# Performance work log

Measured on AMD Instinct MI355X. Metric: run time of the kernel, lower is better.

The kernel has to match this reference:

```python
import jax, jax.numpy as jnp
import numpy as np

N_NODES = 100000
N_EDGES = 1600000
D = 128

def setup_inputs() -> dict:
    key = jax.random.key(0)
    k1, k2, k3, k4 = jax.random.split(key, 4)
    x = jax.random.normal(k1, (N_NODES, D), dtype=jnp.float32)
    edge_index = jax.random.randint(k2, (2, N_EDGES), 0, N_NODES, dtype=jnp.int64)
    eps = jnp.zeros((1,), dtype=jnp.float32)
    W1 = jax.random.normal(k3, (D, D), dtype=jnp.float32) * (1.0 / np.sqrt(D))
    b1 = jnp.zeros((D,), dtype=jnp.float32)
    W2 = jax.random.normal(k4, (D, D), dtype=jnp.float32) * (1.0 / np.sqrt(D))
    b2 = jnp.zeros((D,), dtype=jnp.float32)
    return {"x": x, "edge_index": edge_index, "eps": eps,
            "W1": W1, "b1": b1, "W2": W2, "b2": b2}

def reference(x, edge_index, eps, W1, b1, W2, b2):
    src, dst = edge_index[0], edge_index[1]
    # spmm: sum of neighbor features h_j for each destination node i
    agg = jax.ops.segment_sum(x[src], dst, num_segments=N_NODES)  # [N, D]
    out = (1.0 + eps[0]) * x + agg
    # apply_func: 2-layer MLP (GIN paper)
    h = jax.nn.relu(out @ W1 + b1)
    return h @ W2 + b2
```

## Files before the change

### kernel.cpp

```cpp
#include <hip/hip_runtime.h>

#define D 128
#define BSHIFT 7
#define NSUB 8
#define SUBCAP 384
#define CAP 2560
#define LDSPITCH 136

#define NBMAX 784
#define LCAP 16
#define FCH 8
#define NBIN 256

typedef __attribute__((ext_vector_type(8))) short bf16x8;
typedef __attribute__((ext_vector_type(4))) float f32x4;
typedef __attribute__((ext_vector_type(2))) float f32x2;
typedef __attribute__((ext_vector_type(4))) unsigned int u32x4;

__device__ __forceinline__ unsigned short f2bf(float f) {
    union { float f; unsigned int u; } c; c.f = f;
    return (unsigned short)((c.u + 0x7FFFu + ((c.u >> 16) & 1u)) >> 16);
}

__global__ __launch_bounds__(512) void zerocur(int* __restrict__ cur, int ncur)
{
    int gid = blockIdx.x * 512 + threadIdx.x;
    if (gid < ncur) cur[gid] = 0;
}

__global__ __launch_bounds__(512) void conv_bin(
    const float* __restrict__ x, unsigned short* __restrict__ xb,
    const float* __restrict__ W1, unsigned short* __restrict__ W1t,
    const float* __restrict__ W2, unsigned short* __restrict__ W2t,
    const int* __restrict__ ei, int* __restrict__ cur,
    int* __restrict__ pairs, int E, int nbuck, int total4)
{
    __shared__ int lbuf[NBMAX * LCAP];
    __shared__ int lcnt[NBMAX];

    int tid = threadIdx.x;

    if (blockIdx.x >= NBIN) {
        int base = (blockIdx.x - NBIN) * 1024 + tid;
        #pragma unroll
        for (int t = 0; t < 2; ++t) {
            int gid = base + t * 512;
            if (gid < total4) {
                float4 v = ((const float4*)x)[gid];
                ushort4 o;
                o.x = f2bf(v.x); o.y = f2bf(v.y);
                o.z = f2bf(v.z); o.w = f2bf(v.w);
                ((ushort4*)xb)[gid] = o;
            } else {
                int r = gid - total4;
                if (r < 16384) {
                    int n = r >> 7, k = r & 127;
                    W1t[n * 128 + k] = f2bf(W1[k * 128 + n]);
                } else {
                    r -= 16384;
                    if (r < 16384) {
                        int n = r >> 7, k = r & 127;
                        W2t[n * 128 + k] = f2bf(W2[k * 128 + n]);
                    }
                }
            }
        }
        return;
    }

    int slice = blockIdx.x & (NSUB - 1);
    int epb = (E + NBIN - 1) / NBIN;
    int start = blockIdx.x * epb;
    int end = min(start + epb, E);

    for (int b = tid; b < nbuck; b += 512) lcnt[b] = 0;
    __syncthreads();

    for (int base = start; base < end; base += 512) {
        int gid = base + tid;
        if (gid < end) {
            int d = __builtin_nontemporal_load(&ei[E + gid]);
            int s = __builtin_nontemporal_load(&ei[gid]);
            int b = d >> BSHIFT;
            int val = ((d & 127) << 17) | s;
            int pos = atomicAdd(&lcnt[b], 1);
            if (pos < LCAP) {
                lbuf[b * LCAP + pos] = val;
            } else {
                int sb = b * NSUB + slice;
                int gp = atomicAdd(&cur[sb], 1);
                if (gp < SUBCAP) pairs[(size_t)sb * SUBCAP + gp] = val;
            }
        }
        __syncthreads();
        for (int b = tid; b < nbuck; b += 512) {
            int c = min(lcnt[b], LCAP);
            int nf = (c / FCH) * FCH;
            if (nf > 0) {
                int sb = b * NSUB + slice;
                int gbase = atomicAdd(&cur[sb], nf);
                int* dst = pairs + (size_t)sb * SUBCAP + gbase;
                if ((gbase & 3) == 0 && gbase + nf <= SUBCAP) {
                    #pragma unroll
                    for (int i = 0; i < LCAP; i += 4) {
                        if (i >= nf) break;
                        *(int4*)(dst + i) = *(int4*)(lbuf + b * LCAP + i);
                    }
                } else {
                    for (int i = 0; i < nf; ++i)
                        if (gbase + i < SUBCAP) dst[i] = lbuf[b * LCAP + i];
                }
                int rem = c - nf;
                for (int i = 0; i < rem; ++i)
                    lbuf[b * LCAP + i] = lbuf[b * LCAP + nf + i];
                lcnt[b] = rem;
            } else {
                lcnt[b] = c;
            }
        }
        __syncthreads();
    }

    for (int b = tid; b < nbuck; b += 512) {
        int c = min(lcnt[b], LCAP);
        if (c > 0) {
            int sb = b * NSUB + slice;
            int gbase = atomicAdd(&cur[sb], c);
            for (int i = 0; i < c; ++i)
                if (gbase + i < SUBCAP)
                    pairs[(size_t)sb * SUBCAP + gbase + i] = lbuf[b * LCAP + i];
        }
    }
}

__global__ __launch_bounds__(256) void local_fill(
    const int* __restrict__ cur, const int* __restrict__ pairs,
    int* __restrict__ csr, int* __restrict__ rs, int N)
{
    __shared__ int ldata[CAP];
    __shared__ int outsrc[CAP];
    __shared__ int lcnt[128], lofs[128], lincl[128];
    __shared__ int red[256];

    int b = blockIdx.x;
    int tid = threadIdx.x;
    int node0 = b << BSHIFT;

    int pacc = 0;
    for (int i = tid; i < b * NSUB; i += 256) pacc += min(cur[i], SUBCAP);
    red[tid] = pacc;
    __syncthreads();
    for (int s = 128; s > 0; s >>= 1) {
        if (tid < s) red[tid] += red[tid + s];
        __syncthreads();
    }
    int base = red[0];

    int off = 0;
    #pragma unroll
    for (int s = 0; s < NSUB; ++s) {
        int c = min(cur[b * NSUB + s], SUBCAP);
        const int* pp = pairs + (size_t)(b * NSUB + s) * SUBCAP;
        for (int i = tid; i < c && off + i < CAP; i += 256)
            ldata[off + i] = pp[i];
        off += c;
    }
    int cnt = min(off, CAP);
    __syncthreads();

    if (tid < 128) lcnt[tid] = 0;
    __syncthreads();
    for (int i = tid; i < cnt; i += 256)
        atomicAdd(&lcnt[ldata[i] >> 17], 1);
    __syncthreads();

    if (tid < 128) lincl[tid] = lcnt[tid];
    __syncthreads();
    for (int off2 = 1; off2 < 128; off2 <<= 1) {
        int t = 0;
        if (tid < 128 && tid >= off2) t = lincl[tid - off2];
        __syncthreads();
        if (tid < 128) lincl[tid] += t;
        __syncthreads();
    }
    if (tid < 128) lofs[tid] = lincl[tid] - lcnt[tid];
    __syncthreads();

    for (int i = tid; i < cnt; i += 256) {
        int v = ldata[i];
        int p = atomicAdd(&lofs[v >> 17], 1);
        outsrc[p] = v & 0x1FFFF;
    }
    __syncthreads();

    for (int i = tid; i < cnt; i += 256)
        csr[base + i] = outsrc[i];
    int nn = N - node0; if (nn > 128) nn = 128;
    if (tid < nn) rs[node0 + tid] = base + lincl[tid];
}

__global__ __launch_bounds__(256, 3) void mlp_gather(
    const unsigned short* __restrict__ xb, const float* __restrict__ epsp,
    const int* __restrict__ rs, const int* __restrict__ csr,
    const unsigned short* __restrict__ W1t, const float* __restrict__ b1,
    const unsigned short* __restrict__ W2t, const float* __restrict__ b2,
    float* __restrict__ out, int N)
{
    __shared__ unsigned short Wl[128 * LDSPITCH];
    __shared__ unsigned short Al[64 * LDSPITCH];

    int tid = threadIdx.x;
    int row0 = blockIdx.x * 64;

    for (int i = tid; i < 128 * 16; i += 256) {
        int r = i >> 4, cc = i & 15;
        ((int4*)(Wl + r * LDSPITCH))[cc] = ((const int4*)(W1t + r * 128))[cc];
    }

    {
        int sub  = tid >> 5;
        int lane = threadIdx.x & 31;
        int hi   = lane >> 4;
        int c16  = lane & 15;
        int boff = c16 * 8;
        float ep1 = 1.0f + epsp[0];

        for (int nn = 0; nn < 8; ++nn) {
            int r = nn * 8 + sub;
            int node = row0 + r;
            if (node >= N) {
                if (hi == 0) {
                    u32x4 z = {0u, 0u, 0u, 0u};
                    *(u32x4*)(Al + r * LDSPITCH + boff) = z;
                }
                continue;
            }
            int start = (node == 0) ? 0 : rs[node - 1];
            int end   = rs[node];

            f32x2 acc[4];
            {
                u32x4 xr = *(const u32x4*)(xb + (size_t)node * D + boff);
                f32x2 z2 = {0.f, 0.f};
                #pragma unroll
                for (int e = 0; e < 4; ++e) {
                    unsigned int w = xr[e];
                    f32x2 t;
                    t.x = __uint_as_float(w << 16);
                    t.y = __uint_as_float(w & 0xFFFF0000u);
                    acc[e] = hi ? z2 : (ep1 * t);
                }
            }

            #define ACC8(v)                                                 \
                {                                                           \
                    _Pragma("unroll")                                       \
                    for (int e = 0; e < 4; ++e) {                           \
                        unsigned int w = (v)[e];                            \
                        f32x2 t;                                            \
                        t.x = __uint_as_float(w << 16);                     \
                        t.y = __uint_as_float(w & 0xFFFF0000u);             \
                        acc[e] += t;                                        \
                    }                                                       \
                }

            int j = start;
            for (; j + 8 <= end; j += 8) {
                int i0 = csr[j + hi],     i1 = csr[j + 2 + hi];
                int i2 = csr[j + 4 + hi], i3 = csr[j + 6 + hi];
                u32x4 v0 = *(const u32x4*)(xb + (size_t)i0 * D + boff);
                u32x4 v1 = *(const u32x4*)(xb + (size_t)i1 * D + boff);
                u32x4 v2 = *(const u32x4*)(xb + (size_t)i2 * D + boff);
                u32x4 v3 = *(const u32x4*)(xb + (size_t)i3 * D + boff);
                ACC8(v0); ACC8(v1); ACC8(v2); ACC8(v3);
            }
            if (j < end) {
                int lim = end - 1;
                int e0 = j + hi, e1 = j + 2 + hi;
                int e2 = j + 4 + hi, e3 = j + 6 + hi;
                int s0 = csr[min(e0, lim)], s1 = csr[min(e1, lim)];
                int s2 = csr[min(e2, lim)], s3 = csr[min(e3, lim)];
                u32x4 v0 = *(const u32x4*)(xb + (size_t)s0 * D + boff);
                u32x4 v1 = *(const u32x4*)(xb + (size_t)s1 * D + boff);
                u32x4 v2 = *(const u32x4*)(xb + (size_t)s2 * D + boff);
                u32x4 v3 = *(const u32x4*)(xb + (size_t)s3 * D + boff);
                unsigned int m0 = (e0 < end) ? 0xFFFFFFFFu : 0u;
                unsigned int m1 = (e1 < end) ? 0xFFFFFFFFu : 0u;
                unsigned int m2 = (e2 < end) ? 0xFFFFFFFFu : 0u;
                unsigned int m3 = (e3 < end) ? 0xFFFFFFFFu : 0u;
                #pragma unroll
                for (int e = 0; e < 4; ++e) {
                    v0[e] &= m0; v1[e] &= m1; v2[e] &= m2; v3[e] &= m3;
                }
                ACC8(v0); ACC8(v1); ACC8(v2); ACC8(v3);
            }
            #undef ACC8

            #pragma unroll
            for (int e = 0; e < 4; ++e) {
                acc[e].x += __shfl_xor(acc[e].x, 16);
                acc[e].y += __shfl_xor(acc[e].y, 16);
            }

            if (hi == 0) {
                u32x4 o;
                #pragma unroll
                for (int e = 0; e < 4; ++e) {
                    unsigned int lo = f2bf(acc[e].x);
                    unsigned int hf = f2bf(acc[e].y);
                    o[e] = lo | (hf << 16);
                }
                *(u32x4*)(Al + r * LDSPITCH + boff) = o;
            }
        }
    }
    __syncthreads();

    int wave = tid >> 6, lane = tid & 63;
    int l16 = lane & 15, lq = lane >> 4;

    f32x4 acc[8];
    #pragma unroll
    for (int t = 0; t < 8; ++t) acc[t] = (f32x4){0.f, 0.f, 0.f, 0.f};

    int arow = wave * 16 + l16;
    #pragma unroll
    for (int kk = 0; kk < 4; ++kk) {
        int k0 = kk * 32 + lq * 8;
        bf16x8 a = *(const bf16x8*)(Al + arow * LDSPITCH + k0);
        #pragma unroll
        for (int t = 0; t < 8; ++t) {
            bf16x8 b = *(const bf16x8*)(Wl + (t * 16 + l16) * LDSPITCH + k0);
            acc[t] = __builtin_amdgcn_mfma_f32_16x16x32_bf16(a, b, acc[t], 0, 0, 0);
        }
    }
    __syncthreads();

    for (int i = tid; i < 128 * 16; i += 256) {
        int r = i >> 4, cc = i & 15;
        ((int4*)(Wl + r * LDSPITCH))[cc] = ((const int4*)(W2t + r * 128))[cc];
    }
    #pragma unroll
    for (int t = 0; t < 8; ++t) {
        int col = t * 16 + l16;
        float bv = b1[col];
        #pragma unroll
        for (int r = 0; r < 4; ++r) {
            int row = wave * 16 + lq * 4 + r;
            float v = fmaxf(acc[t][r] + bv, 0.0f);
            Al[row * LDSPITCH + col] = f2bf(v);
        }
    }
    __syncthreads();

    #pragma unroll
    for (int t = 0; t < 8; ++t) acc[t] = (f32x4){0.f, 0.f, 0.f, 0.f};
    #pragma unroll
    for (int kk = 0; kk < 4; ++kk) {
        int k0 = kk * 32 + lq * 8;
        bf16x8 a = *(const bf16x8*)(Al + arow * LDSPITCH + k0);
        #pragma unroll
        for (int t = 0; t < 8; ++t) {
            bf16x8 b = *(const bf16x8*)(Wl + (t * 16 + l16) * LDSPITCH + k0);
            acc[t] = __builtin_amdgcn_mfma_f32_16x16x32_bf16(a, b, acc[t], 0, 0, 0);
        }
    }

    #pragma unroll
    for (int t = 0; t < 8; ++t) {
        int col = t * 16 + l16;
        float bv = b2[col];
        #pragma unroll
        for (int r = 0; r < 4; ++r) {
            int row = row0 + wave * 16 + lq * 4 + r;
            if (row >= N) continue;
            out[(size_t)row * 128 + col] = acc[t][r] + bv;
        }
    }
}

extern "C" void kernel_launch(void* const* d_in, const int* in_sizes, int n_in,
                              void* d_out, int out_size, void* d_ws, size_t ws_size,
                              hipStream_t stream) {
    const float* x   = (const float*)d_in[0];
    const int*   ei  = (const int*)d_in[1];
    const float* eps = (const float*)d_in[2];
    const float* W1  = (const float*)d_in[3];
    const float* b1  = (const float*)d_in[4];
    const float* W2  = (const float*)d_in[5];
    const float* b2  = (const float*)d_in[6];
    float* out = (float*)d_out;

    int E = in_sizes[1] / 2;
    int N = in_sizes[0] / D;
    int nbuck = (N + 127) >> BSHIFT;
    int ncur = nbuck * NSUB;

    char* ws = (char*)d_ws;
    int* cur   = (int*)(ws);
    int* rs    = (int*)(ws + 32768);
    int* pairs = (int*)(ws + 434176);
    int* csr   = (int*)(ws + 10044416);
    unsigned short* xb  = (unsigned short*)(ws + 16445440);
    unsigned short* W1t = (unsigned short*)(ws + 67647488);
    unsigned short* W2t = (unsigned short*)(ws + 67680256);

    int total4 = N * D / 4;
    int convitems = total4 + 32768;
    int nconv = (convitems + 1023) / 1024;

    zerocur<<<(ncur + 511) / 512, 512, 0, stream>>>(cur, ncur);
    conv_bin<<<NBIN + nconv, 512, 0, stream>>>(
        x, xb, W1, W1t, W2, W2t, ei, cur, pairs, E, nbuck, total4);
    local_fill<<<nbuck, 256, 0, stream>>>(cur, pairs, csr, rs, N);

    int gemm_blocks = (N + 63) / 64;
    mlp_gather<<<gemm_blocks, 256, 0, stream>>>(
        xb, eps, rs, csr, W1t, b1, W2t, b2, out, N);
}
```

Before: 256.5 us.

## Double threads per gather-MLP block and unroll neighbor gather to sixteen edges

The fused gather+MLP kernel now runs 512 threads per 64-row block instead of 256. Each 32-lane group handles 4 nodes instead of 8, and the two MFMA passes are split so each wave computes half the output columns. The neighbor gather loop is unrolled to 16 edges per iteration to keep more loads in flight. This aims to raise memory-level parallelism in the latency-bound gather, at the cost of more register pressure under launch_bounds(512,4) and fewer MFMAs per wave.

```diff
diff --git a/kernel.cpp b/kernel.cpp
--- a/kernel.cpp
+++ b/kernel.cpp
@@ -199,7 +199,7 @@
     if (tid < nn) rs[node0 + tid] = base + lincl[tid];
 }
 
-__global__ __launch_bounds__(256, 3) void mlp_gather(
+__global__ __launch_bounds__(512, 4) void mlp_gather512(
     const unsigned short* __restrict__ xb, const float* __restrict__ epsp,
     const int* __restrict__ rs, const int* __restrict__ csr,
     const unsigned short* __restrict__ W1t, const float* __restrict__ b1,
@@ -212,21 +212,21 @@
     int tid = threadIdx.x;
     int row0 = blockIdx.x * 64;
 
-    for (int i = tid; i < 128 * 16; i += 256) {
+    for (int i = tid; i < 128 * 16; i += 512) {
         int r = i >> 4, cc = i & 15;
         ((int4*)(Wl + r * LDSPITCH))[cc] = ((const int4*)(W1t + r * 128))[cc];
     }
 
     {
         int sub  = tid >> 5;
-        int lane = threadIdx.x & 31;
+        int lane = tid & 31;
         int hi   = lane >> 4;
         int c16  = lane & 15;
         int boff = c16 * 8;
         float ep1 = 1.0f + epsp[0];
 
-        for (int nn = 0; nn < 8; ++nn) {
-            int r = nn * 8 + sub;
+        for (int nn = 0; nn < 4; ++nn) {
+            int r = nn * 16 + sub;
             int node = row0 + r;
             if (node >= N) {
                 if (hi == 0) {
@@ -265,7 +265,23 @@
                 }
 
             int j = start;
-            for (; j + 8 <= end; j += 8) {
+            for (; j + 16 <= end; j += 16) {
+                int i0 = csr[j      + hi], i1 = csr[j +  2 + hi];
+                int i2 = csr[j +  4 + hi], i3 = csr[j +  6 + hi];
+                int i4 = csr[j +  8 + hi], i5 = csr[j + 10 + hi];
+                int i6 = csr[j + 12 + hi], i7 = csr[j + 14 + hi];
+                u32x4 v0 = *(const u32x4*)(xb + (size_t)i0 * D + boff);
+                u32x4 v1 = *(const u32x4*)(xb + (size_t)i1 * D + boff);
+                u32x4 v2 = *(const u32x4*)(xb + (size_t)i2 * D + boff);
+                u32x4 v3 = *(const u32x4*)(xb + (size_t)i3 * D + boff);
+                u32x4 v4 = *(const u32x4*)(xb + (size_t)i4 * D + boff);
+                u32x4 v5 = *(const u32x4*)(xb + (size_t)i5 * D + boff);
+                u32x4 v6 = *(const u32x4*)(xb + (size_t)i6 * D + boff);
+                u32x4 v7 = *(const u32x4*)(xb + (size_t)i7 * D + boff);
+                ACC8(v0); ACC8(v1); ACC8(v2); ACC8(v3);
+                ACC8(v4); ACC8(v5); ACC8(v6); ACC8(v7);
+            }
+            if (j + 8 <= end) {
                 int i0 = csr[j + hi],     i1 = csr[j + 2 + hi];
                 int i2 = csr[j + 4 + hi], i3 = csr[j + 6 + hi];
                 u32x4 v0 = *(const u32x4*)(xb + (size_t)i0 * D + boff);
@@ -273,6 +289,7 @@
                 u32x4 v2 = *(const u32x4*)(xb + (size_t)i2 * D + boff);
                 u32x4 v3 = *(const u32x4*)(xb + (size_t)i3 * D + boff);
                 ACC8(v0); ACC8(v1); ACC8(v2); ACC8(v3);
+                j += 8;
             }
             if (j < end) {
                 int lim = end - 1;
@@ -318,63 +335,67 @@
 
     int wave = tid >> 6, lane = tid & 63;
     int l16 = lane & 15, lq = lane >> 4;
-
-    f32x4 acc[8];
-    #pragma unroll
-    for (int t = 0; t < 8; ++t) acc[t] = (f32x4){0.f, 0.f, 0.f, 0.f};
-
-    int arow = wave * 16 + l16;
+    int g = wave >> 1;
+    int h = wave & 1;
+    int arow = g * 16 + l16;
+
+    f32x4 acc[4];
+    #pragma unroll
+    for (int t = 0; t < 4; ++t) acc[t] = (f32x4){0.f, 0.f, 0.f, 0.f};
+
     #pragma unroll
     for (int kk = 0; kk < 4; ++kk) {
         int k0 = kk * 32 + lq * 8;
         bf16x8 a = *(const bf16x8*)(Al + arow * LDSPITCH + k0);
         #pragma unroll
-        for (int t = 0; t < 8; ++t) {
+        for (int tt = 0; tt < 4; ++tt) {
+            int t = h * 4 + tt;
             bf16x8 b = *(const bf16x8*)(Wl + (t * 16 + l16) * LDSPITCH + k0);
-            acc[t] = __builtin_amdgcn_mfma_f32_16x16x32_bf16(a, b, acc[t], 0, 0, 0);
-        }
-    }
-    __syncthreads();
-
-    for (int i = tid; i < 128 * 16; i += 256) {
+            acc[tt] = __builtin_amdgcn_mfma_f32_16x16x32_bf16(a, b, acc[tt], 0, 0, 0);
+        }
+    }
+    __syncthreads();
+
+    for (int i = tid; i < 128 * 16; i += 512) {
         int r = i >> 4, cc = i & 15;
         ((int4*)(Wl + r * LDSPITCH))[cc] = ((const int4*)(W2t + r * 128))[cc];
     }
     #pragma unroll
-    for (int t = 0; t < 8; ++t) {
-        int col = t * 16 + l16;
+    for (int tt = 0; tt < 4; ++tt) {
+        int col = (h * 4 + tt) * 16 + l16;
         float bv = b1[col];
         #pragma unroll
         for (int r = 0; r < 4; ++r) {
-            int row = wave * 16 + lq * 4 + r;
-            float v = fmaxf(acc[t][r] + bv, 0.0f);
+            int row = g * 16 + lq * 4 + r;
+            float v = fmaxf(acc[tt][r] + bv, 0.0f);
             Al[row * LDSPITCH + col] = f2bf(v);
         }
     }
     __syncthreads();
 
     #pragma unroll
-    for (int t = 0; t < 8; ++t) acc[t] = (f32x4){0.f, 0.f, 0.f, 0.f};
+    for (int t = 0; t < 4; ++t) acc[t] = (f32x4){0.f, 0.f, 0.f, 0.f};
     #pragma unroll
     for (int kk = 0; kk < 4; ++kk) {
         int k0 = kk * 32 + lq * 8;
         bf16x8 a = *(const bf16x8*)(Al + arow * LDSPITCH + k0);
         #pragma unroll
-        for (int t = 0; t < 8; ++t) {
+        for (int tt = 0; tt < 4; ++tt) {
+            int t = h * 4 + tt;
             bf16x8 b = *(const bf16x8*)(Wl + (t * 16 + l16) * LDSPITCH + k0);
-            acc[t] = __builtin_amdgcn_mfma_f32_16x16x32_bf16(a, b, acc[t], 0, 0, 0);
-        }
-    }
-
-    #pragma unroll
-    for (int t = 0; t < 8; ++t) {
-        int col = t * 16 + l16;
+            acc[tt] = __builtin_amdgcn_mfma_f32_16x16x32_bf16(a, b, acc[tt], 0, 0, 0);
+        }
+    }
+
+    #pragma unroll
+    for (int tt = 0; tt < 4; ++tt) {
+        int col = (h * 4 + tt) * 16 + l16;
         float bv = b2[col];
         #pragma unroll
         for (int r = 0; r < 4; ++r) {
-            int row = row0 + wave * 16 + lq * 4 + r;
+            int row = row0 + g * 16 + lq * 4 + r;
             if (row >= N) continue;
-            out[(size_t)row * 128 + col] = acc[t][r] + bv;
+            out[(size_t)row * 128 + col] = acc[tt][r] + bv;
         }
     }
 }
@@ -415,6 +436,6 @@
     local_fill<<<nbuck, 256, 0, stream>>>(cur, pairs, csr, rs, N);
 
     int gemm_blocks = (N + 63) / 64;
-    mlp_gather<<<gemm_blocks, 256, 0, stream>>>(
+    mlp_gather512<<<gemm_blocks, 512, 0, stream>>>(
         xb, eps, rs, csr, W1t, b1, W2t, b2, out, N);
 }
```

Result: faster. 239.3 us (-6.7%).
